# Kernel tuning notes

Measured on AMD Instinct MI355X. Metric: run time of the kernel, lower is better.

Reference implementation:

```python
import jax, jax.numpy as jnp
import numpy as np
import math


def setup_inputs() -> dict:
    key = jax.random.key(0)
    k1, k2 = jax.random.split(key)
    x = jax.random.normal(k1, (16, 512, 32, 32), dtype=jnp.float32)
    gamma = jax.random.normal(k2, (1,), dtype=jnp.float32)  # learned scale (init 0 in torch; randomized here)
    beta = 0.5 * jnp.ones((1,), dtype=jnp.float32)          # learned blend (init 0.5)
    return {"x": x, "gamma": gamma, "beta": beta}


def reference(x, gamma, beta):
    # x: (B, C, H, W)
    B, C, H, W = x.shape
    N = H * W
    Xf = x.reshape(B, C, N)  # proj_query / proj_value

    # ave_I = (1/N) * (I - (1/N) * ones(N,N)); X @ ave_I == (X - mean_N(X)) / N exactly.
    Xc = Xf - jnp.mean(Xf, axis=2, keepdims=True)
    scale = 1.0 / (N * math.sqrt(N))
    # sigma = proj_query @ ave_I @ proj_key / sqrt(N)  -> (B, C, C)
    sigma = jnp.einsum('bcn,bdn->bcd', Xc, Xf) * scale

    # energy = proj_query @ proj_key  -> (B, C, C)
    energy = jnp.einsum('bcn,bdn->bcd', Xf, Xf)
    energy_new = jnp.max(energy, axis=-1, keepdims=True) - energy

    b = beta[0]
    attention = b * jax.nn.softmax(sigma, axis=-1) + (1.0 - b) * jax.nn.softmax(energy_new, axis=-1)

    out = jnp.einsum('bcd,bdn->bcn', attention, Xf).reshape(B, C, H, W)
    out = gamma[0] * out + x
    return out
```

## Files before the change

kernel.cpp:

```cpp
#include <hip/hip_runtime.h>

typedef unsigned short u16;
typedef __bf16 bf16x8 __attribute__((ext_vector_type(8)));
typedef float f32x4 __attribute__((ext_vector_type(4)));

#define AS1 __attribute__((address_space(1)))
#define AS3 __attribute__((address_space(3)))

#define BB 16
#define CC 512
#define NN 1024

__device__ __forceinline__ void async16(void* lds, const void* g) {
  __builtin_amdgcn_global_load_lds((AS1 void*)g, (AS3 void*)lds, 16, 0, 0);
}

__device__ __forceinline__ u16 f2bf(float f) {
  unsigned u = __float_as_uint(f);
  return (u16)((u + 0x7FFFu + ((u >> 16) & 1u)) >> 16);
}
__device__ __forceinline__ float bf2f(u16 h) {
  return __uint_as_float(((unsigned)h) << 16);
}

__device__ __forceinline__ float wredSum(float v) {
  for (int m = 32; m >= 1; m >>= 1) v += __shfl_xor(v, m, 64);
  return v;
}
__device__ __forceinline__ float wredMin(float v) {
  for (int m = 32; m >= 1; m >>= 1) v = fminf(v, __shfl_xor(v, m, 64));
  return v;
}
__device__ __forceinline__ float wredMax(float v) {
  for (int m = 32; m >= 1; m >>= 1) v = fmaxf(v, __shfl_xor(v, m, 64));
  return v;
}

template <int ROWS, int T>
__device__ __forceinline__ void stageT(u16* lds, const u16* src, size_t ld, int t) {
#pragma unroll
  for (int i = 0; i < ROWS * 8 / T; ++i) {
    int f = i * T + t;
    int row = f >> 3;
    int c8 = f & 7;
    int sc = (c8 ^ (row & 7)) * 8;
    async16(&lds[(size_t)f * 8], src + (size_t)row * ld + sc);
  }
}

__device__ __forceinline__ bf16x8 ldsfrag(const u16* lds, int row, int k0) {
  return *(const bf16x8*)&lds[row * 64 + (k0 ^ ((row & 7) * 8))];
}

__global__ __launch_bounds__(256) void k_prepT(const float* __restrict__ x,
                                               u16* __restrict__ xhi,
                                               u16* __restrict__ xlo,
                                               u16* __restrict__ xt,
                                               float* __restrict__ mu) {
  int lid = blockIdx.x;
  int sw = (lid & 7) * 32 + (lid >> 3);
  int b = sw >> 4;
  int c0 = (sw & 15) * 32;
  int t = threadIdx.x;
  int row = t >> 3;
  int col4 = t & 7;
  __shared__ u16 tr[2][64][40];

  const float* xb = x + ((size_t)b * CC + c0) * NN;
  u16* hb = xhi + ((size_t)b * CC + c0) * NN;
  u16* lb = xlo + ((size_t)b * CC + c0) * NN;
  u16* tb = xt + (size_t)b * NN * CC + c0;

  float sum = 0.f;
  int wkey = col4 * 4;
  for (int nt = 0; nt < 16; ++nt) {
    u16(*tbuf)[40] = tr[nt & 1];
#pragma unroll
    for (int s = 0; s < 2; ++s) {
      int cc4 = col4 + 8 * s;
      size_t off = (size_t)row * NN + nt * 64 + cc4 * 4;
      float4 v = *(const float4*)&xb[off];
      sum += v.x + v.y + v.z + v.w;
      ushort4 h, l;
      h.x = f2bf(v.x); l.x = f2bf(v.x - bf2f(h.x));
      h.y = f2bf(v.y); l.y = f2bf(v.y - bf2f(h.y));
      h.z = f2bf(v.z); l.z = f2bf(v.z - bf2f(h.z));
      h.w = f2bf(v.w); l.w = f2bf(v.w - bf2f(h.w));
      *(ushort4*)&hb[off] = h;
      *(ushort4*)&lb[off] = l;
      int csw = row ^ wkey;
      tbuf[cc4 * 4 + 0][csw] = h.x;
      tbuf[cc4 * 4 + 1][csw] = h.y;
      tbuf[cc4 * 4 + 2][csw] = h.z;
      tbuf[cc4 * 4 + 3][csw] = h.w;
    }
    __syncthreads();
    int np = t >> 2, cs = t & 3;
    int rkey = ((np >> 2) & 7) * 4;
#pragma unroll
    for (int s2 = 0; s2 < 2; ++s2) {
      int cl = cs * 4 + s2 * 16;
      *(ushort4*)&tb[(size_t)(nt * 64 + np) * CC + cl] =
          *(ushort4*)&tbuf[np][cl ^ rkey];
    }
  }
  sum += __shfl_xor(sum, 1, 64);
  sum += __shfl_xor(sum, 2, 64);
  sum += __shfl_xor(sum, 4, 64);
  if ((t & 7) == 0) mu[(size_t)b * CC + c0 + row] = sum * (1.0f / (float)NN);
}

__global__ __launch_bounds__(256, 2) void k_gemm1(const u16* __restrict__ xhi,
                                                  const u16* __restrict__ xlo,
                                                  float* __restrict__ M) {
  int lid = blockIdx.x;
  int sw = (lid & 7) * 64 + (lid >> 3);
  int b = sw >> 5;
  int r = sw & 31;
  int by = r >> 3;
  int bx = r & 7;

  __shared__ u16 lds[2 * 16384];
  int t = threadIdx.x;
  int lane = t & 63, w = t >> 6;
  int wr = (w >> 1) * 64;
  int wc = (w & 1) * 32;
  int fr = lane & 15, fk = (lane >> 4) * 8;

  const u16* Ab = xhi + ((size_t)b * CC + by * 128) * NN;
  const u16* Bh = xhi + ((size_t)b * CC + bx * 64) * NN;
  const u16* Bl = xlo + ((size_t)b * CC + bx * 64) * NN;

  f32x4 accH[4][2], accL[4][2];
#pragma unroll
  for (int m = 0; m < 4; ++m)
#pragma unroll
    for (int n = 0; n < 2; ++n) { accH[m][n] = (f32x4)(0.0f); accL[m][n] = (f32x4)(0.0f); }

  stageT<128, 256>(lds, Ab, NN, t);
  stageT<64, 256>(lds + 8192, Bh, NN, t);
  stageT<64, 256>(lds + 12288, Bl, NN, t);
  __syncthreads();

  int cur = 0;
  for (int ks = 0; ks < NN; ks += 64) {
    if (ks + 64 < NN) {
      u16* nb = lds + (cur ^ 1) * 16384;
      stageT<128, 256>(nb, Ab + ks + 64, NN, t);
      stageT<64, 256>(nb + 8192, Bh + ks + 64, NN, t);
      stageT<64, 256>(nb + 12288, Bl + ks + 64, NN, t);
    }
    const u16* cb = lds + cur * 16384;
#pragma unroll
    for (int kk = 0; kk < 2; ++kk) {
      bf16x8 af[4], bh[2], bl[2];
#pragma unroll
      for (int m = 0; m < 4; ++m) af[m] = ldsfrag(cb, wr + m * 16 + fr, kk * 32 + fk);
#pragma unroll
      for (int n = 0; n < 2; ++n) {
        bh[n] = ldsfrag(cb + 8192, wc + n * 16 + fr, kk * 32 + fk);
        bl[n] = ldsfrag(cb + 12288, wc + n * 16 + fr, kk * 32 + fk);
      }
#pragma unroll
      for (int m = 0; m < 4; ++m)
#pragma unroll
        for (int n = 0; n < 2; ++n) {
          accH[m][n] = __builtin_amdgcn_mfma_f32_16x16x32_bf16(af[m], bh[n], accH[m][n], 0, 0, 0);
          accL[m][n] = __builtin_amdgcn_mfma_f32_16x16x32_bf16(af[m], bl[n], accL[m][n], 0, 0, 0);
        }
    }
    __syncthreads();
    cur ^= 1;
  }

  float* Mb = M + ((size_t)b * CC + by * 128) * CC + bx * 64;
  int orow = wr + (lane >> 4) * 4;
  int ocol = wc + (lane & 15);
#pragma unroll
  for (int m = 0; m < 4; ++m)
#pragma unroll
    for (int n = 0; n < 2; ++n)
#pragma unroll
      for (int q = 0; q < 4; ++q)
        Mb[(size_t)(orow + m * 16 + q) * CC + ocol + n * 16] =
            0.5f * accH[m][n][q] + accL[m][n][q];
}

__global__ __launch_bounds__(256) void k_att(const float* __restrict__ M,
                                             const float* __restrict__ mu,
                                             const float* __restrict__ beta_p,
                                             u16* __restrict__ att) {
  __shared__ float pt[32][513];
  int lid = blockIdx.x;
  int sw = (lid & 7) * 32 + (lid >> 3);
  int b = sw >> 4;
  int c0 = (sw & 15) * 32;
  int t = threadIdx.x;
  const float* Mb = M + (size_t)b * CC * CC;

  int cb = (t & 7) * 4;
  for (int d = t >> 3; d < CC; d += 32) {
    float4 v = *(const float4*)&Mb[(size_t)d * CC + c0 + cb];
    pt[cb + 0][d] = v.x;
    pt[cb + 1][d] = v.y;
    pt[cb + 2][d] = v.z;
    pt[cb + 3][d] = v.w;
  }
  __syncthreads();

  int lane = t & 63, w = t >> 6;
  const float* mub = mu + b * CC;
  float bta = *beta_p;

  for (int i = 0; i < 8; ++i) {
    int cl = w * 8 + i;
    int c = c0 + cl;
    const float* r0 = Mb + (size_t)c * CC;
    float muc = mub[c];

    float e[8], mud[8];
#pragma unroll
    for (int j = 0; j < 8; ++j) {
      int d = lane + j * 64;
      e[j] = r0[d] + pt[cl][d];
      mud[j] = mub[d];
    }
    float emin = fminf(fminf(fminf(e[0], e[1]), fminf(e[2], e[3])),
                       fminf(fminf(e[4], e[5]), fminf(e[6], e[7])));
    emin = wredMin(emin);
    float pe[8], sum_e = 0.f;
#pragma unroll
    for (int j = 0; j < 8; ++j) { pe[j] = __expf(emin - e[j]); sum_e += pe[j]; }
    sum_e = wredSum(sum_e);

    float sg[8];
#pragma unroll
    for (int j = 0; j < 8; ++j)
      sg[j] = (e[j] - (float)NN * muc * mud[j]) * (1.0f / 32768.0f);
    float smax = fmaxf(fmaxf(fmaxf(sg[0], sg[1]), fmaxf(sg[2], sg[3])),
                       fmaxf(fmaxf(sg[4], sg[5]), fmaxf(sg[6], sg[7])));
    smax = wredMax(smax);
    float ps[8], sum_s = 0.f;
#pragma unroll
    for (int j = 0; j < 8; ++j) { ps[j] = __expf(sg[j] - smax); sum_s += ps[j]; }
    sum_s = wredSum(sum_s);

    float we = (1.0f - bta) / sum_e;
    float wsc = bta / sum_s;
    u16* arow = att + ((size_t)b * CC + c) * CC;
#pragma unroll
    for (int j = 0; j < 8; ++j)
      arow[lane + j * 64] = f2bf(ps[j] * wsc + pe[j] * we);
  }
}

__global__ __launch_bounds__(256, 2) void k_gemm2(const u16* __restrict__ att,
                                                  const u16* __restrict__ xt,
                                                  const float* __restrict__ x,
                                                  const float* __restrict__ gamma_p,
                                                  float* __restrict__ out) {
  int lid = blockIdx.x;
  int sw = (lid & 7) * 64 + (lid >> 3);
  int b = sw >> 5;
  int r = sw & 31;
  int by = r >> 3;
  int bx = r & 7;

  __shared__ u16 lds[2 * 16384];
  int t = threadIdx.x;
  int lane = t & 63, w = t >> 6;
  int wr = (w >> 1) * 64, wc = (w & 1) * 64;
  int fr = lane & 15, fk = (lane >> 4) * 8;

  const u16* Ab = att + ((size_t)b * CC + by * 128) * CC;
  const u16* Bb = xt + ((size_t)b * NN + bx * 128) * CC;

  f32x4 acc[4][4];
#pragma unroll
  for (int m = 0; m < 4; ++m)
#pragma unroll
    for (int n = 0; n < 4; ++n) acc[m][n] = (f32x4)(0.0f);

  stageT<128, 256>(lds, Ab, CC, t);
  stageT<128, 256>(lds + 8192, Bb, CC, t);
  __syncthreads();

  int cur = 0;
  for (int ks = 0; ks < CC; ks += 64) {
    if (ks + 64 < CC) {
      u16* nb = lds + (cur ^ 1) * 16384;
      stageT<128, 256>(nb, Ab + ks + 64, CC, t);
      stageT<128, 256>(nb + 8192, Bb + ks + 64, CC, t);
    }
    const u16* cb = lds + cur * 16384;
#pragma unroll
    for (int kk = 0; kk < 2; ++kk) {
      bf16x8 af[4], bg[4];
#pragma unroll
      for (int m = 0; m < 4; ++m) af[m] = ldsfrag(cb, wr + m * 16 + fr, kk * 32 + fk);
#pragma unroll
      for (int n = 0; n < 4; ++n) bg[n] = ldsfrag(cb + 8192, wc + n * 16 + fr, kk * 32 + fk);
#pragma unroll
      for (int m = 0; m < 4; ++m)
#pragma unroll
        for (int n = 0; n < 4; ++n)
          acc[m][n] = __builtin_amdgcn_mfma_f32_16x16x32_bf16(af[m], bg[n], acc[m][n], 0, 0, 0);
    }
    __syncthreads();
    cur ^= 1;
  }

  float g = *gamma_p;
  const float* xb = x + ((size_t)b * CC + by * 128) * NN + bx * 128;
  float* ob = out + ((size_t)b * CC + by * 128) * NN + bx * 128;
  int orow = wr + (lane >> 4) * 4;
  int ocol = wc + (lane & 15);
#pragma unroll
  for (int m = 0; m < 4; ++m)
#pragma unroll
    for (int n = 0; n < 4; ++n)
#pragma unroll
      for (int q = 0; q < 4; ++q) {
        size_t rr = (size_t)(orow + m * 16 + q) * NN + ocol + n * 16;
        ob[rr] = g * acc[m][n][q] + xb[rr];
      }
}

extern "C" void kernel_launch(void* const* d_in, const int* in_sizes, int n_in,
                              void* d_out, int out_size, void* d_ws, size_t ws_size,
                              hipStream_t stream) {
  const float* x = (const float*)d_in[0];
  const float* gamma = (const float*)d_in[1];
  const float* beta = (const float*)d_in[2];
  float* out = (float*)d_out;

  constexpr size_t BCN = (size_t)BB * CC * NN;
  constexpr size_t BCC = (size_t)BB * CC * CC;
  u16* xhi = (u16*)d_ws;
  u16* xlo = xhi + BCN;
  u16* xt = xlo + BCN;
  float* mu = (float*)(xt + BCN);
  float* M = mu + (size_t)BB * CC;
  u16* att = xhi;

  k_prepT<<<256, 256, 0, stream>>>(x, xhi, xlo, xt, mu);
  k_gemm1<<<512, 256, 0, stream>>>(xhi, xlo, M);
  k_att<<<256, 256, 0, stream>>>(M, mu, beta, att);
  k_gemm2<<<512, 256, 0, stream>>>(att, xt, x, gamma, out);
}
```

Before: 72.40 us.

## Switch to fp16 single-pass Gram matrix, dropping hi/lo bf16 split

Replaces the split bf16 hi/lo representation with a single fp16 copy of x, so the Gram GEMM runs one MFMA stream instead of two and the lo buffer is neither written nor read. Gram tiles become 128x128 with half the blocks. The attention kernel now reads E directly rather than symmetrising M with a transposed LDS copy. All GEMMs use f16 MFMA. This trades the extra precision of the error-compensated split for fewer MFMAs and less memory traffic, and risks fp16 range or accuracy issues in the energy softmax, where large values (around N) amplify rounding error.

```diff
diff --git a/kernel.cpp b/kernel.cpp
--- a/kernel.cpp
+++ b/kernel.cpp
@@ -1,7 +1,7 @@
 #include <hip/hip_runtime.h>
 
 typedef unsigned short u16;
-typedef __bf16 bf16x8 __attribute__((ext_vector_type(8)));
+typedef _Float16 f16x8 __attribute__((ext_vector_type(8)));
 typedef float f32x4 __attribute__((ext_vector_type(4)));
 
 #define AS1 __attribute__((address_space(1)))
@@ -15,12 +15,9 @@
   __builtin_amdgcn_global_load_lds((AS1 void*)g, (AS3 void*)lds, 16, 0, 0);
 }
 
-__device__ __forceinline__ u16 f2bf(float f) {
-  unsigned u = __float_as_uint(f);
-  return (u16)((u + 0x7FFFu + ((u >> 16) & 1u)) >> 16);
-}
-__device__ __forceinline__ float bf2f(u16 h) {
-  return __uint_as_float(((unsigned)h) << 16);
+__device__ __forceinline__ u16 f2h(float f) {
+  _Float16 h = (_Float16)f;
+  return __builtin_bit_cast(u16, h);
 }
 
 __device__ __forceinline__ float wredSum(float v) {
@@ -48,13 +45,12 @@
   }
 }
 
-__device__ __forceinline__ bf16x8 ldsfrag(const u16* lds, int row, int k0) {
-  return *(const bf16x8*)&lds[row * 64 + (k0 ^ ((row & 7) * 8))];
+__device__ __forceinline__ f16x8 ldsfrag(const u16* lds, int row, int k0) {
+  return *(const f16x8*)&lds[row * 64 + (k0 ^ ((row & 7) * 8))];
 }
 
 __global__ __launch_bounds__(256) void k_prepT(const float* __restrict__ x,
-                                               u16* __restrict__ xhi,
-                                               u16* __restrict__ xlo,
+                                               u16* __restrict__ xh,
                                                u16* __restrict__ xt,
                                                float* __restrict__ mu) {
   int lid = blockIdx.x;
@@ -67,8 +63,7 @@
   __shared__ u16 tr[2][64][40];
 
   const float* xb = x + ((size_t)b * CC + c0) * NN;
-  u16* hb = xhi + ((size_t)b * CC + c0) * NN;
-  u16* lb = xlo + ((size_t)b * CC + c0) * NN;
+  u16* hb = xh + ((size_t)b * CC + c0) * NN;
   u16* tb = xt + (size_t)b * NN * CC + c0;
 
   float sum = 0.f;
@@ -81,13 +76,9 @@
       size_t off = (size_t)row * NN + nt * 64 + cc4 * 4;
       float4 v = *(const float4*)&xb[off];
       sum += v.x + v.y + v.z + v.w;
-      ushort4 h, l;
-      h.x = f2bf(v.x); l.x = f2bf(v.x - bf2f(h.x));
-      h.y = f2bf(v.y); l.y = f2bf(v.y - bf2f(h.y));
-      h.z = f2bf(v.z); l.z = f2bf(v.z - bf2f(h.z));
-      h.w = f2bf(v.w); l.w = f2bf(v.w - bf2f(h.w));
+      ushort4 h;
+      h.x = f2h(v.x); h.y = f2h(v.y); h.z = f2h(v.z); h.w = f2h(v.w);
       *(ushort4*)&hb[off] = h;
-      *(ushort4*)&lb[off] = l;
       int csw = row ^ wkey;
       tbuf[cc4 * 4 + 0][csw] = h.x;
       tbuf[cc4 * 4 + 1][csw] = h.y;
@@ -110,36 +101,32 @@
   if ((t & 7) == 0) mu[(size_t)b * CC + c0 + row] = sum * (1.0f / (float)NN);
 }
 
-__global__ __launch_bounds__(256, 2) void k_gemm1(const u16* __restrict__ xhi,
-                                                  const u16* __restrict__ xlo,
-                                                  float* __restrict__ M) {
+__global__ __launch_bounds__(256, 2) void k_gemm1(const u16* __restrict__ xh,
+                                                  float* __restrict__ E) {
   int lid = blockIdx.x;
-  int sw = (lid & 7) * 64 + (lid >> 3);
-  int b = sw >> 5;
-  int r = sw & 31;
-  int by = r >> 3;
-  int bx = r & 7;
+  int sw = (lid & 7) * 32 + (lid >> 3);
+  int b = sw >> 4;
+  int r = sw & 15;
+  int by = r >> 2;
+  int bx = r & 3;
 
   __shared__ u16 lds[2 * 16384];
   int t = threadIdx.x;
   int lane = t & 63, w = t >> 6;
-  int wr = (w >> 1) * 64;
-  int wc = (w & 1) * 32;
+  int wr = (w >> 1) * 64, wc = (w & 1) * 64;
   int fr = lane & 15, fk = (lane >> 4) * 8;
 
-  const u16* Ab = xhi + ((size_t)b * CC + by * 128) * NN;
-  const u16* Bh = xhi + ((size_t)b * CC + bx * 64) * NN;
-  const u16* Bl = xlo + ((size_t)b * CC + bx * 64) * NN;
-
-  f32x4 accH[4][2], accL[4][2];
+  const u16* Ab = xh + ((size_t)b * CC + by * 128) * NN;
+  const u16* Bb = xh + ((size_t)b * CC + bx * 128) * NN;
+
+  f32x4 acc[4][4];
 #pragma unroll
   for (int m = 0; m < 4; ++m)
 #pragma unroll
-    for (int n = 0; n < 2; ++n) { accH[m][n] = (f32x4)(0.0f); accL[m][n] = (f32x4)(0.0f); }
+    for (int n = 0; n < 4; ++n) acc[m][n] = (f32x4)(0.0f);
 
   stageT<128, 256>(lds, Ab, NN, t);
-  stageT<64, 256>(lds + 8192, Bh, NN, t);
-  stageT<64, 256>(lds + 12288, Bl, NN, t);
+  stageT<128, 256>(lds + 8192, Bb, NN, t);
   __syncthreads();
 
   int cur = 0;
@@ -147,82 +134,62 @@
     if (ks + 64 < NN) {
       u16* nb = lds + (cur ^ 1) * 16384;
       stageT<128, 256>(nb, Ab + ks + 64, NN, t);
-      stageT<64, 256>(nb + 8192, Bh + ks + 64, NN, t);
-      stageT<64, 256>(nb + 12288, Bl + ks + 64, NN, t);
+      stageT<128, 256>(nb + 8192, Bb + ks + 64, NN, t);
     }
     const u16* cb = lds + cur * 16384;
 #pragma unroll
     for (int kk = 0; kk < 2; ++kk) {
-      bf16x8 af[4], bh[2], bl[2];
+      f16x8 af[4], bg[4];
 #pragma unroll
       for (int m = 0; m < 4; ++m) af[m] = ldsfrag(cb, wr + m * 16 + fr, kk * 32 + fk);
 #pragma unroll
-      for (int n = 0; n < 2; ++n) {
-        bh[n] = ldsfrag(cb + 8192, wc + n * 16 + fr, kk * 32 + fk);
-        bl[n] = ldsfrag(cb + 12288, wc + n * 16 + fr, kk * 32 + fk);
-      }
+      for (int n = 0; n < 4; ++n) bg[n] = ldsfrag(cb + 8192, wc + n * 16 + fr, kk * 32 + fk);
 #pragma unroll
       for (int m = 0; m < 4; ++m)
 #pragma unroll
-        for (int n = 0; n < 2; ++n) {
-          accH[m][n] = __builtin_amdgcn_mfma_f32_16x16x32_bf16(af[m], bh[n], accH[m][n], 0, 0, 0);
-          accL[m][n] = __builtin_amdgcn_mfma_f32_16x16x32_bf16(af[m], bl[n], accL[m][n], 0, 0, 0);
-        }
+        for (int n = 0; n < 4; ++n)
+          acc[m][n] = __builtin_amdgcn_mfma_f32_16x16x32_f16(af[m], bg[n], acc[m][n], 0, 0, 0);
     }
     __syncthreads();
     cur ^= 1;
   }
 
-  float* Mb = M + ((size_t)b * CC + by * 128) * CC + bx * 64;
+  float* Eb = E + ((size_t)b * CC + by * 128) * CC + bx * 128;
   int orow = wr + (lane >> 4) * 4;
   int ocol = wc + (lane & 15);
 #pragma unroll
   for (int m = 0; m < 4; ++m)
 #pragma unroll
-    for (int n = 0; n < 2; ++n)
+    for (int n = 0; n < 4; ++n)
 #pragma unroll
       for (int q = 0; q < 4; ++q)
-        Mb[(size_t)(orow + m * 16 + q) * CC + ocol + n * 16] =
-            0.5f * accH[m][n][q] + accL[m][n][q];
-}
-
-__global__ __launch_bounds__(256) void k_att(const float* __restrict__ M,
+        Eb[(size_t)(orow + m * 16 + q) * CC + ocol + n * 16] = acc[m][n][q];
+}
+
+__global__ __launch_bounds__(256) void k_att(const float* __restrict__ E,
                                              const float* __restrict__ mu,
                                              const float* __restrict__ beta_p,
                                              u16* __restrict__ att) {
-  __shared__ float pt[32][513];
   int lid = blockIdx.x;
   int sw = (lid & 7) * 32 + (lid >> 3);
   int b = sw >> 4;
   int c0 = (sw & 15) * 32;
   int t = threadIdx.x;
-  const float* Mb = M + (size_t)b * CC * CC;
-
-  int cb = (t & 7) * 4;
-  for (int d = t >> 3; d < CC; d += 32) {
-    float4 v = *(const float4*)&Mb[(size_t)d * CC + c0 + cb];
-    pt[cb + 0][d] = v.x;
-    pt[cb + 1][d] = v.y;
-    pt[cb + 2][d] = v.z;
-    pt[cb + 3][d] = v.w;
-  }
-  __syncthreads();
-
   int lane = t & 63, w = t >> 6;
+  const float* Eb = E + (size_t)b * CC * CC;
   const float* mub = mu + b * CC;
   float bta = *beta_p;
 
   for (int i = 0; i < 8; ++i) {
-    int cl = w * 8 + i;
-    int c = c0 + cl;
-    const float* r0 = Mb + (size_t)c * CC;
+    int c = c0 + w * 8 + i;
+    const float* r0 = Eb + (size_t)c * CC;
     float muc = mub[c];
 
     float e[8], mud[8];
 #pragma unroll
     for (int j = 0; j < 8; ++j) {
       int d = lane + j * 64;
-      e[j] = r0[d] + pt[cl][d];
+      e[j] = r0[d];
       mud[j] = mub[d];
     }
     float emin = fminf(fminf(fminf(e[0], e[1]), fminf(e[2], e[3])),
@@ -250,7 +217,7 @@
     u16* arow = att + ((size_t)b * CC + c) * CC;
 #pragma unroll
     for (int j = 0; j < 8; ++j)
-      arow[lane + j * 64] = f2bf(ps[j] * wsc + pe[j] * we);
+      arow[lane + j * 64] = f2h(ps[j] * wsc + pe[j] * we);
   }
 }
 
@@ -295,7 +262,7 @@
     const u16* cb = lds + cur * 16384;
 #pragma unroll
     for (int kk = 0; kk < 2; ++kk) {
-      bf16x8 af[4], bg[4];
+      f16x8 af[4], bg[4];
 #pragma unroll
       for (int m = 0; m < 4; ++m) af[m] = ldsfrag(cb, wr + m * 16 + fr, kk * 32 + fk);
 #pragma unroll
@@ -304,7 +271,7 @@
       for (int m = 0; m < 4; ++m)
 #pragma unroll
         for (int n = 0; n < 4; ++n)
-          acc[m][n] = __builtin_amdgcn_mfma_f32_16x16x32_bf16(af[m], bg[n], acc[m][n], 0, 0, 0);
+          acc[m][n] = __builtin_amdgcn_mfma_f32_16x16x32_f16(af[m], bg[n], acc[m][n], 0, 0, 0);
     }
     __syncthreads();
     cur ^= 1;
@@ -336,15 +303,14 @@
 
   constexpr size_t BCN = (size_t)BB * CC * NN;
   constexpr size_t BCC = (size_t)BB * CC * CC;
-  u16* xhi = (u16*)d_ws;
-  u16* xlo = xhi + BCN;
-  u16* xt = xlo + BCN;
+  u16* xh = (u16*)d_ws;
+  u16* xt = xh + BCN;
   float* mu = (float*)(xt + BCN);
-  float* M = mu + (size_t)BB * CC;
-  u16* att = xhi;
-
-  k_prepT<<<256, 256, 0, stream>>>(x, xhi, xlo, xt, mu);
-  k_gemm1<<<512, 256, 0, stream>>>(xhi, xlo, M);
-  k_att<<<256, 256, 0, stream>>>(M, mu, beta, att);
+  float* E = mu + (size_t)BB * CC;
+  u16* att = xh;
+
+  k_prepT<<<256, 256, 0, stream>>>(x, xh, xt, mu);
+  k_gemm1<<<256, 256, 0, stream>>>(xh, E);
+  k_att<<<256, 256, 0, stream>>>(E, mu, beta, att);
   k_gemm2<<<512, 256, 0, stream>>>(att, xt, x, gamma, out);
 }
```

Result: faster. 69.86 us (-3.5%).
